# Optimization experiments

Measured on AMD Instinct MI355X. Metric: run time of the kernel, lower is better.

Reference implementation:

```python
import jax, jax.numpy as jnp
import numpy as np

NUM_FEATURES = 128
NUM_FILTERS = 128

def setup_inputs() -> dict:
    key = jax.random.key(0)
    k1, k2, k3, k4, k5 = jax.random.split(key, 5)
    B, N, F = 4, 2048, NUM_FEATURES
    x = jax.random.normal(k1, (B, N, F), dtype=jnp.float32)
    A = jax.random.normal(k2, (B, N, N), dtype=jnp.float32)
    # Conv1D(num_filters, kernel_size=1, use_bias=False) == per-node linear F -> filters
    W = jax.random.normal(k3, (F, NUM_FILTERS), dtype=jnp.float32) * (1.0 / np.sqrt(F))
    # self.a: Conv1D(1, kernel_size=1) with bias == linear filters -> 1 (shared for x_i and x_j)
    a_w = jax.random.normal(k4, (NUM_FILTERS, 1), dtype=jnp.float32) * (1.0 / np.sqrt(NUM_FILTERS))
    a_b = jax.random.normal(k5, (1,), dtype=jnp.float32) * 0.01
    bias = jnp.zeros((NUM_FILTERS,), dtype=jnp.float32)
    return {"x": x, "A": A, "W": W, "a_w": a_w, "a_b": a_b, "bias": bias}

def reference(x, A, W, a_w, a_b, bias):
    # project features: [B,N,F] @ [F,Ff] -> [B,N,Ff]
    h = jnp.einsum('bnf,fg->bng', x, W)
    # shared attention projection (x_i and x_j use the same layer): [B,N,1]
    s = jnp.einsum('bng,go->bno', h, a_w) + a_b
    # additive scores s_i + s_j^T -> [B,N,N]
    e = s + jnp.swapaxes(s, 1, 2)
    e = jnp.where(e >= 0, e, 0.2 * e)  # LeakyReLU(0.2)
    attn = jax.nn.softmax(e + A, axis=-1)
    out = jnp.einsum('bij,bjg->big', attn, h) + bias
    return out
```

## Files before the change

kernel.cpp:

```cpp
#include <hip/hip_runtime.h>
#include <hip/hip_bf16.h>
#include <stdint.h>

#define BB 4
#define NN 2048
#define FF 128

typedef __attribute__((ext_vector_type(8))) short bf16x8;
typedef __attribute__((ext_vector_type(4))) float f32x4;

__device__ inline unsigned pk_bf16(float a, float b) {
    union { float f; unsigned u; } x, y;
    x.f = a; y.f = b;
    unsigned xu = x.u + (0x7fffu + ((x.u >> 16) & 1u));
    unsigned yu = y.u + (0x7fffu + ((y.u >> 16) & 1u));
    return (xu >> 16) | (yu & 0xffff0000u);
}

#define XT_P 136
#define WT_P 136

__global__ __launch_bounds__(256) void k1_proj(
    const float* __restrict__ x, const float* __restrict__ W,
    const float* __restrict__ a_w, const float* __restrict__ a_b,
    uint16_t* __restrict__ Ht, float* __restrict__ s_out)
{
    __shared__ uint16_t xt[16 * XT_P];
    __shared__ uint16_t Wt[128 * WT_P];
    __shared__ float sredw[4 * 16];

    const int t = threadIdx.x;
    const int w = t >> 6, l = t & 63;
    const int m16 = l & 15, q = l >> 4;
    const int b = blockIdx.x >> 7;
    const int n0 = (blockIdx.x & 127) << 4;

    const int c4 = (t & 31) * 4, kh = (t >> 5) * 16;
    float4 wr0[8], wr1[8];
    #pragma unroll
    for (int kk = 0; kk < 8; ++kk) {
        const int k = kh + 2 * kk;
        wr0[kk] = *(const float4*)(W + (size_t)k * 128 + c4);
        wr1[kk] = *(const float4*)(W + (size_t)(k + 1) * 128 + c4);
    }
    {
        const int row = t >> 4, c0 = (t & 15) * 8;
        const float* xr = x + ((size_t)(b * NN + n0 + row)) * FF + c0;
        const float4 v0 = *(const float4*)xr;
        const float4 v1 = *(const float4*)(xr + 4);
        unsigned* dst = (unsigned*)(xt + row * XT_P + c0);
        dst[0] = pk_bf16(v0.x, v0.y); dst[1] = pk_bf16(v0.z, v0.w);
        dst[2] = pk_bf16(v1.x, v1.y); dst[3] = pk_bf16(v1.z, v1.w);
    }
    #pragma unroll
    for (int kk = 0; kk < 8; ++kk) {
        const int k = kh + 2 * kk;
        *(unsigned*)(Wt + (c4 + 0) * WT_P + k) = pk_bf16(wr0[kk].x, wr1[kk].x);
        *(unsigned*)(Wt + (c4 + 1) * WT_P + k) = pk_bf16(wr0[kk].y, wr1[kk].y);
        *(unsigned*)(Wt + (c4 + 2) * WT_P + k) = pk_bf16(wr0[kk].z, wr1[kk].z);
        *(unsigned*)(Wt + (c4 + 3) * WT_P + k) = pk_bf16(wr0[kk].w, wr1[kk].w);
    }
    const int g0 = (2 * w) * 16 + m16, g1 = (2 * w + 1) * 16 + m16;
    const float aw0 = a_w[g0], aw1 = a_w[g1];
    __syncthreads();

    f32x4 acc0 = {}, acc1 = {};
    bf16x8 af[4];
    #pragma unroll
    for (int dk = 0; dk < 4; ++dk)
        af[dk] = *(const bf16x8*)(xt + m16 * XT_P + dk * 32 + q * 8);
    #pragma unroll
    for (int dk = 0; dk < 4; ++dk) {
        bf16x8 b0 = *(const bf16x8*)(Wt + g0 * WT_P + dk * 32 + q * 8);
        bf16x8 b1 = *(const bf16x8*)(Wt + g1 * WT_P + dk * 32 + q * 8);
        acc0 = __builtin_amdgcn_mfma_f32_16x16x32_bf16(af[dk], b0, acc0, 0, 0, 0);
        acc1 = __builtin_amdgcn_mfma_f32_16x16x32_bf16(af[dk], b1, acc1, 0, 0, 0);
    }

    float sp[4];
    #pragma unroll
    for (int r = 0; r < 4; ++r) sp[r] = acc0[r] * aw0 + acc1[r] * aw1;
    #pragma unroll
    for (int off = 1; off < 16; off <<= 1)
        #pragma unroll
        for (int r = 0; r < 4; ++r) sp[r] += __shfl_xor(sp[r], off, 64);
    if (m16 == 0) {
        #pragma unroll
        for (int r = 0; r < 4; ++r) sredw[w * 16 + q * 4 + r] = sp[r];
    }
    {
        uint2 o0 = { pk_bf16(acc0[0], acc0[1]), pk_bf16(acc0[2], acc0[3]) };
        uint2 o1 = { pk_bf16(acc1[0], acc1[1]), pk_bf16(acc1[2], acc1[3]) };
        *(uint2*)(Ht + ((size_t)(b * 128 + g0)) * NN + n0 + q * 4) = o0;
        *(uint2*)(Ht + ((size_t)(b * 128 + g1)) * NN + n0 + q * 4) = o1;
    }
    __syncthreads();
    if (t < 16)
        s_out[b * NN + n0 + t] = sredw[t] + sredw[16 + t] + sredw[32 + t] + sredw[48 + t] + a_b[0];
}

#define JS 8
#define IRND 8

__global__ __launch_bounds__(256, 2) void k2_attn(
    const float* __restrict__ A, const uint16_t* __restrict__ Ht,
    const float* __restrict__ s, uint16_t* __restrict__ po,
    float* __restrict__ prs)
{
    __shared__ float Opw[4][16 * 132];
    __shared__ float rsw[4][16];

    const int t = threadIdx.x;
    const int w = t >> 6, l = t & 63;
    const int m16 = l & 15, q = l >> 4;

    const int bx = blockIdx.x;
    const int js = bx & 7;
    const int is = (bx >> 3) & 15;
    const int b  = bx >> 7;
    const int j0 = js * 256;
    const int ibase = is * 128;

    const float* sb = s + b * NN;
    const float* Ab = A + (size_t)b * NN * NN;
    const uint16_t* Hb = Ht + (size_t)b * FF * NN;

    const int jc0 = j0 + w * 32 + q * 8;
    const int jc1 = j0 + (w + 4) * 32 + q * 8;

    float4 sj00 = *(const float4*)(sb + jc0);
    float4 sj01 = *(const float4*)(sb + jc0 + 4);
    float4 sj10 = *(const float4*)(sb + jc1);
    float4 sj11 = *(const float4*)(sb + jc1 + 4);

    bf16x8 hf0[8], hf1[8];
    #pragma unroll
    for (int gt = 0; gt < 8; ++gt) {
        const uint16_t* hp = Hb + (size_t)(gt * 16 + m16) * NN;
        hf0[gt] = *(const bf16x8*)(hp + jc0);
        hf1[gt] = *(const bf16x8*)(hp + jc1);
    }

    const float* Ar = Ab + (size_t)(ibase + m16) * NN;
    float4 a00 = *(const float4*)(Ar + jc0);
    float4 a01 = *(const float4*)(Ar + jc0 + 4);
    float4 a10 = *(const float4*)(Ar + jc1);
    float4 a11 = *(const float4*)(Ar + jc1 + 4);
    float si = sb[ibase + m16];

    const size_t slice = (size_t)(js * BB + b);

    for (int r = 0; r < IRND; ++r) {
        const int i0r = ibase + r * 16;
        const int i0n = ibase + ((r + 1) & (IRND - 1)) * 16;

        const float* An = Ab + (size_t)(i0n + m16) * NN;
        float4 n00 = *(const float4*)(An + jc0);
        float4 n01 = *(const float4*)(An + jc0 + 4);
        float4 n10 = *(const float4*)(An + jc1);
        float4 n11 = *(const float4*)(An + jc1 + 4);
        const float sin_ = sb[i0n + m16];

        const float svv[16] = {sj00.x,sj00.y,sj00.z,sj00.w, sj01.x,sj01.y,sj01.z,sj01.w,
                               sj10.x,sj10.y,sj10.z,sj10.w, sj11.x,sj11.y,sj11.z,sj11.w};
        const float avv[16] = {a00.x,a00.y,a00.z,a00.w, a01.x,a01.y,a01.z,a01.w,
                               a10.x,a10.y,a10.z,a10.w, a11.x,a11.y,a11.z,a11.w};
        float pv[16]; float rs = 0.f;
        #pragma unroll
        for (int j = 0; j < 16; ++j) {
            float e = si + svv[j];
            e = fmaxf(e, 0.2f * e);
            pv[j] = __expf(e + avv[j]);
            rs += pv[j];
        }
        union { unsigned u[4]; bf16x8 v; } fa0, fa1;
        #pragma unroll
        for (int j = 0; j < 4; ++j) {
            fa0.u[j] = pk_bf16(pv[2 * j], pv[2 * j + 1]);
            fa1.u[j] = pk_bf16(pv[8 + 2 * j], pv[9 + 2 * j]);
        }

        f32x4 acc[8];
        #pragma unroll
        for (int gt = 0; gt < 8; ++gt) {
            f32x4 z = {0.f, 0.f, 0.f, 0.f};
            z = __builtin_amdgcn_mfma_f32_16x16x32_bf16(fa0.v, hf0[gt], z, 0, 0, 0);
            acc[gt] = __builtin_amdgcn_mfma_f32_16x16x32_bf16(fa1.v, hf1[gt], z, 0, 0, 0);
        }

        rs += __shfl_xor(rs, 16, 64);
        rs += __shfl_xor(rs, 32, 64);
        if (q == 0) rsw[w][m16] = rs;

        #pragma unroll
        for (int gt = 0; gt < 8; ++gt)
            #pragma unroll
            for (int rr = 0; rr < 4; ++rr)
                Opw[w][(q * 4 + rr) * 132 + gt * 16 + m16] = acc[gt][rr];
        asm volatile("s_waitcnt lgkmcnt(0)\n\ts_barrier" ::: "memory");

        {
            const int row = t >> 4, k8 = (t & 15) * 8;
            float v[8] = {0.f,0.f,0.f,0.f,0.f,0.f,0.f,0.f};
            #pragma unroll
            for (int sl = 0; sl < 4; ++sl) {
                float4 u0 = *(const float4*)&Opw[sl][row * 132 + k8];
                float4 u1 = *(const float4*)&Opw[sl][row * 132 + k8 + 4];
                v[0] += u0.x; v[1] += u0.y; v[2] += u0.z; v[3] += u0.w;
                v[4] += u1.x; v[5] += u1.y; v[6] += u1.z; v[7] += u1.w;
            }
            unsigned* op = (unsigned*)(po + ((slice * NN + i0r + row) * FF + k8));
            op[0] = pk_bf16(v[0], v[1]); op[1] = pk_bf16(v[2], v[3]);
            op[2] = pk_bf16(v[4], v[5]); op[3] = pk_bf16(v[6], v[7]);
            if (t < 16)
                prs[slice * NN + i0r + t] = rsw[0][t] + rsw[1][t] + rsw[2][t] + rsw[3][t];
        }
        asm volatile("s_waitcnt lgkmcnt(0)\n\ts_barrier" ::: "memory");

        a00 = n00; a01 = n01; a10 = n10; a11 = n11; si = sin_;
    }
}

__global__ __launch_bounds__(256) void k3_red(
    const uint16_t* __restrict__ po, const float* __restrict__ prs,
    const float* __restrict__ bias, float* __restrict__ out)
{
    const int idx = blockIdx.x * 256 + threadIdx.x;
    const int g = idx & 127;
    const int i = (idx >> 7) & (NN - 1);
    const int b = idx >> 18;
    float sum = 0.f, rsum = 0.f;
    #pragma unroll
    for (int js = 0; js < JS; ++js) {
        const size_t base = (size_t)(js * BB + b) * NN + i;
        union { unsigned u; float f; } cv;
        cv.u = ((unsigned)po[base * FF + g]) << 16;
        sum += cv.f;
        rsum += prs[base];
    }
    out[idx] = sum / rsum + bias[g];
}

extern "C" void kernel_launch(void* const* d_in, const int* in_sizes, int n_in,
                              void* d_out, int out_size, void* d_ws, size_t ws_size,
                              hipStream_t stream) {
    const float* x    = (const float*)d_in[0];
    const float* A    = (const float*)d_in[1];
    const float* W    = (const float*)d_in[2];
    const float* a_w  = (const float*)d_in[3];
    const float* a_b  = (const float*)d_in[4];
    const float* bias = (const float*)d_in[5];
    float* out = (float*)d_out;

    char* ws = (char*)d_ws;
    uint16_t* Ht = (uint16_t*)ws;
    float* s = (float*)(ws + 2 * 1024 * 1024);
    uint16_t* po = (uint16_t*)(ws + 2 * 1024 * 1024 + 65536);
    float* prs = (float*)(ws + 2 * 1024 * 1024 + 65536 + (size_t)JS * BB * NN * FF * 2);

    k1_proj<<<BB * (NN / 16), 256, 0, stream>>>(x, W, a_w, a_b, Ht, s);
    k2_attn<<<JS * 16 * BB, 256, 0, stream>>>(A, Ht, s, po, prs);
    k3_red<<<(BB * NN * FF) / 256, 256, 0, stream>>>(po, prs, bias, out);
}
```

Baseline: 126.7 us.

## Give each attention block full j range and fuse final reduction, drop k3

Changes the attention kernel split. Each block used to own a 256-column j-slice and 128 rows of i, writing bf16 partials that a third kernel reduced. Each block now owns 16 rows of i across the full j range and accumulates in MFMA registers, then normalizes, adds bias and writes fp32 output directly. This removes the partial-sum workspace traffic, the third launch and the per-round barriers. In exchange the block reloads the H fragments for every j chunk instead of keeping them resident, so H is read 8x more often (from L2). There is also no softmax max subtraction, same as before.

After: 138.7 us. +9.4%, slower.

```diff
diff --git a/kernel.cpp b/kernel.cpp
--- a/kernel.cpp
+++ b/kernel.cpp
@@ -99,13 +99,10 @@
         s_out[b * NN + n0 + t] = sredw[t] + sredw[16 + t] + sredw[32 + t] + sredw[48 + t] + a_b[0];
 }
 
-#define JS 8
-#define IRND 8
-
 __global__ __launch_bounds__(256, 2) void k2_attn(
     const float* __restrict__ A, const uint16_t* __restrict__ Ht,
-    const float* __restrict__ s, uint16_t* __restrict__ po,
-    float* __restrict__ prs)
+    const float* __restrict__ s, const float* __restrict__ bias,
+    float* __restrict__ out)
 {
     __shared__ float Opw[4][16 * 132];
     __shared__ float rsw[4][16];
@@ -114,58 +111,64 @@
     const int w = t >> 6, l = t & 63;
     const int m16 = l & 15, q = l >> 4;
 
-    const int bx = blockIdx.x;
-    const int js = bx & 7;
-    const int is = (bx >> 3) & 15;
-    const int b  = bx >> 7;
-    const int j0 = js * 256;
-    const int ibase = is * 128;
+    const int is = blockIdx.x & 127;
+    const int b  = blockIdx.x >> 7;
+    const int ibase = is * 16;
 
     const float* sb = s + b * NN;
     const float* Ab = A + (size_t)b * NN * NN;
     const uint16_t* Hb = Ht + (size_t)b * FF * NN;
 
-    const int jc0 = j0 + w * 32 + q * 8;
-    const int jc1 = j0 + (w + 4) * 32 + q * 8;
-
-    float4 sj00 = *(const float4*)(sb + jc0);
-    float4 sj01 = *(const float4*)(sb + jc0 + 4);
-    float4 sj10 = *(const float4*)(sb + jc1);
-    float4 sj11 = *(const float4*)(sb + jc1 + 4);
-
-    bf16x8 hf0[8], hf1[8];
-    #pragma unroll
-    for (int gt = 0; gt < 8; ++gt) {
-        const uint16_t* hp = Hb + (size_t)(gt * 16 + m16) * NN;
-        hf0[gt] = *(const bf16x8*)(hp + jc0);
-        hf1[gt] = *(const bf16x8*)(hp + jc1);
-    }
-
+    const float si = sb[ibase + m16];
     const float* Ar = Ab + (size_t)(ibase + m16) * NN;
-    float4 a00 = *(const float4*)(Ar + jc0);
-    float4 a01 = *(const float4*)(Ar + jc0 + 4);
-    float4 a10 = *(const float4*)(Ar + jc1);
-    float4 a11 = *(const float4*)(Ar + jc1 + 4);
-    float si = sb[ibase + m16];
-
-    const size_t slice = (size_t)(js * BB + b);
-
-    for (int r = 0; r < IRND; ++r) {
-        const int i0r = ibase + r * 16;
-        const int i0n = ibase + ((r + 1) & (IRND - 1)) * 16;
-
-        const float* An = Ab + (size_t)(i0n + m16) * NN;
-        float4 n00 = *(const float4*)(An + jc0);
-        float4 n01 = *(const float4*)(An + jc0 + 4);
-        float4 n10 = *(const float4*)(An + jc1);
-        float4 n11 = *(const float4*)(An + jc1 + 4);
-        const float sin_ = sb[i0n + m16];
+
+    const int co = w * 32 + q * 8;
+
+    float4 a00 = *(const float4*)(Ar + co);
+    float4 a01 = *(const float4*)(Ar + co + 4);
+    float4 a10 = *(const float4*)(Ar + co + 128);
+    float4 a11 = *(const float4*)(Ar + co + 132);
+    float4 sj00 = *(const float4*)(sb + co);
+    float4 sj01 = *(const float4*)(sb + co + 4);
+    float4 sj10 = *(const float4*)(sb + co + 128);
+    float4 sj11 = *(const float4*)(sb + co + 132);
+
+    f32x4 acc[8];
+    #pragma unroll
+    for (int gt = 0; gt < 8; ++gt) acc[gt] = (f32x4){0.f, 0.f, 0.f, 0.f};
+    float rs = 0.f;
+
+    #pragma unroll
+    for (int r = 0; r < 8; ++r) {
+        const int jc0 = r * 256 + co;
+        const int jc1 = jc0 + 128;
+
+        bf16x8 hf0[8], hf1[8];
+        #pragma unroll
+        for (int gt = 0; gt < 8; ++gt) {
+            const uint16_t* hp = Hb + (size_t)(gt * 16 + m16) * NN;
+            hf0[gt] = *(const bf16x8*)(hp + jc0);
+            hf1[gt] = *(const bf16x8*)(hp + jc1);
+        }
+
+        float4 n00, n01, n10, n11, t00, t01, t10, t11;
+        if (r < 7) {
+            const int jn = jc0 + 256;
+            n00 = *(const float4*)(Ar + jn);
+            n01 = *(const float4*)(Ar + jn + 4);
+            n10 = *(const float4*)(Ar + jn + 128);
+            n11 = *(const float4*)(Ar + jn + 132);
+            t00 = *(const float4*)(sb + jn);
+            t01 = *(const float4*)(sb + jn + 4);
+            t10 = *(const float4*)(sb + jn + 128);
+            t11 = *(const float4*)(sb + jn + 132);
+        }
 
         const float svv[16] = {sj00.x,sj00.y,sj00.z,sj00.w, sj01.x,sj01.y,sj01.z,sj01.w,
                                sj10.x,sj10.y,sj10.z,sj10.w, sj11.x,sj11.y,sj11.z,sj11.w};
         const float avv[16] = {a00.x,a00.y,a00.z,a00.w, a01.x,a01.y,a01.z,a01.w,
                                a10.x,a10.y,a10.z,a10.w, a11.x,a11.y,a11.z,a11.w};
-        float pv[16]; float rs = 0.f;
+        float pv[16];
         #pragma unroll
         for (int j = 0; j < 16; ++j) {
             float e = si + svv[j];
@@ -180,65 +183,48 @@
             fa1.u[j] = pk_bf16(pv[8 + 2 * j], pv[9 + 2 * j]);
         }
 
-        f32x4 acc[8];
         #pragma unroll
         for (int gt = 0; gt < 8; ++gt) {
-            f32x4 z = {0.f, 0.f, 0.f, 0.f};
-            z = __builtin_amdgcn_mfma_f32_16x16x32_bf16(fa0.v, hf0[gt], z, 0, 0, 0);
-            acc[gt] = __builtin_amdgcn_mfma_f32_16x16x32_bf16(fa1.v, hf1[gt], z, 0, 0, 0);
-        }
-
-        rs += __shfl_xor(rs, 16, 64);
-        rs += __shfl_xor(rs, 32, 64);
-        if (q == 0) rsw[w][m16] = rs;
-
-        #pragma unroll
-        for (int gt = 0; gt < 8; ++gt)
-            #pragma unroll
-            for (int rr = 0; rr < 4; ++rr)
-                Opw[w][(q * 4 + rr) * 132 + gt * 16 + m16] = acc[gt][rr];
-        asm volatile("s_waitcnt lgkmcnt(0)\n\ts_barrier" ::: "memory");
-
-        {
-            const int row = t >> 4, k8 = (t & 15) * 8;
-            float v[8] = {0.f,0.f,0.f,0.f,0.f,0.f,0.f,0.f};
-            #pragma unroll
-            for (int sl = 0; sl < 4; ++sl) {
-                float4 u0 = *(const float4*)&Opw[sl][row * 132 + k8];
-                float4 u1 = *(const float4*)&Opw[sl][row * 132 + k8 + 4];
-                v[0] += u0.x; v[1] += u0.y; v[2] += u0.z; v[3] += u0.w;
-                v[4] += u1.x; v[5] += u1.y; v[6] += u1.z; v[7] += u1.w;
-            }
-            unsigned* op = (unsigned*)(po + ((slice * NN + i0r + row) * FF + k8));
-            op[0] = pk_bf16(v[0], v[1]); op[1] = pk_bf16(v[2], v[3]);
-            op[2] = pk_bf16(v[4], v[5]); op[3] = pk_bf16(v[6], v[7]);
-            if (t < 16)
-                prs[slice * NN + i0r + t] = rsw[0][t] + rsw[1][t] + rsw[2][t] + rsw[3][t];
-        }
-        asm volatile("s_waitcnt lgkmcnt(0)\n\ts_barrier" ::: "memory");
-
-        a00 = n00; a01 = n01; a10 = n10; a11 = n11; si = sin_;
-    }
-}
-
-__global__ __launch_bounds__(256) void k3_red(
-    const uint16_t* __restrict__ po, const float* __restrict__ prs,
-    const float* __restrict__ bias, float* __restrict__ out)
-{
-    const int idx = blockIdx.x * 256 + threadIdx.x;
-    const int g = idx & 127;
-    const int i = (idx >> 7) & (NN - 1);
-    const int b = idx >> 18;
-    float sum = 0.f, rsum = 0.f;
-    #pragma unroll
-    for (int js = 0; js < JS; ++js) {
-        const size_t base = (size_t)(js * BB + b) * NN + i;
-        union { unsigned u; float f; } cv;
-        cv.u = ((unsigned)po[base * FF + g]) << 16;
-        sum += cv.f;
-        rsum += prs[base];
-    }
-    out[idx] = sum / rsum + bias[g];
+            acc[gt] = __builtin_amdgcn_mfma_f32_16x16x32_bf16(fa0.v, hf0[gt], acc[gt], 0, 0, 0);
+            acc[gt] = __builtin_amdgcn_mfma_f32_16x16x32_bf16(fa1.v, hf1[gt], acc[gt], 0, 0, 0);
+        }
+
+        if (r < 7) {
+            a00 = n00; a01 = n01; a10 = n10; a11 = n11;
+            sj00 = t00; sj01 = t01; sj10 = t10; sj11 = t11;
+        }
+    }
+
+    rs += __shfl_xor(rs, 16, 64);
+    rs += __shfl_xor(rs, 32, 64);
+    if (q == 0) rsw[w][m16] = rs;
+    #pragma unroll
+    for (int gt = 0; gt < 8; ++gt)
+        #pragma unroll
+        for (int rr = 0; rr < 4; ++rr)
+            Opw[w][(q * 4 + rr) * 132 + gt * 16 + m16] = acc[gt][rr];
+    __syncthreads();
+
+    {
+        const int row = t >> 4, k8 = (t & 15) * 8;
+        float v[8] = {0.f,0.f,0.f,0.f,0.f,0.f,0.f,0.f};
+        #pragma unroll
+        for (int sl = 0; sl < 4; ++sl) {
+            float4 u0 = *(const float4*)&Opw[sl][row * 132 + k8];
+            float4 u1 = *(const float4*)&Opw[sl][row * 132 + k8 + 4];
+            v[0] += u0.x; v[1] += u0.y; v[2] += u0.z; v[3] += u0.w;
+            v[4] += u1.x; v[5] += u1.y; v[6] += u1.z; v[7] += u1.w;
+        }
+        const float rst = rsw[0][row] + rsw[1][row] + rsw[2][row] + rsw[3][row];
+        const float inv = 1.0f / rst;
+        const float4 b0 = *(const float4*)(bias + k8);
+        const float4 b1 = *(const float4*)(bias + k8 + 4);
+        float4 o0 = { v[0]*inv + b0.x, v[1]*inv + b0.y, v[2]*inv + b0.z, v[3]*inv + b0.w };
+        float4 o1 = { v[4]*inv + b1.x, v[5]*inv + b1.y, v[6]*inv + b1.z, v[7]*inv + b1.w };
+        float* op = out + ((size_t)(b * NN + ibase + row)) * FF + k8;
+        *(float4*)op = o0;
+        *(float4*)(op + 4) = o1;
+    }
 }
 
 extern "C" void kernel_launch(void* const* d_in, const int* in_sizes, int n_in,
@@ -255,10 +241,7 @@
     char* ws = (char*)d_ws;
     uint16_t* Ht = (uint16_t*)ws;
     float* s = (float*)(ws + 2 * 1024 * 1024);
-    uint16_t* po = (uint16_t*)(ws + 2 * 1024 * 1024 + 65536);
-    float* prs = (float*)(ws + 2 * 1024 * 1024 + 65536 + (size_t)JS * BB * NN * FF * 2);
 
     k1_proj<<<BB * (NN / 16), 256, 0, stream>>>(x, W, a_w, a_b, Ht, s);
-    k2_attn<<<JS * 16 * BB, 256, 0, stream>>>(A, Ht, s, po, prs);
-    k3_red<<<(BB * NN * FF) / 256, 256, 0, stream>>>(po, prs, bias, out);
-}
+    k2_attn<<<128 * BB, 256, 0, stream>>>(A, Ht, s, bias, out);
+}
```

## Halve i-rows per attention block and vectorize the final reduction

Applied to the files above, without the earlier changes.

The attention kernel now processes 4 row rounds of 16 (64 rows) per block instead of 8 (128 rows), doubling the grid to 1024 blocks for better occupancy and load balance across CUs. This costs twice as many reloads of the per-block H fragments. The reduction kernel now handles 8 features per thread with 16-byte loads and stores, multiplies by a reciprocal instead of dividing, and launches one eighth as many threads. The odd 'acc[gt] = z' expression inside the MFMA call is redundant but harmless.

After: 128.0 us. No clear change (+1.0%).

```diff
diff --git a/kernel.cpp b/kernel.cpp
--- a/kernel.cpp
+++ b/kernel.cpp
@@ -100,7 +100,7 @@
 }
 
 #define JS 8
-#define IRND 8
+#define IRND 4
 
 __global__ __launch_bounds__(256, 2) void k2_attn(
     const float* __restrict__ A, const uint16_t* __restrict__ Ht,
@@ -116,10 +116,10 @@
 
     const int bx = blockIdx.x;
     const int js = bx & 7;
-    const int is = (bx >> 3) & 15;
-    const int b  = bx >> 7;
+    const int is = (bx >> 3) & 31;
+    const int b  = bx >> 8;
     const int j0 = js * 256;
-    const int ibase = is * 128;
+    const int ibase = is * 64;
 
     const float* sb = s + b * NN;
     const float* Ab = A + (size_t)b * NN * NN;
@@ -185,7 +185,7 @@
         for (int gt = 0; gt < 8; ++gt) {
             f32x4 z = {0.f, 0.f, 0.f, 0.f};
             z = __builtin_amdgcn_mfma_f32_16x16x32_bf16(fa0.v, hf0[gt], z, 0, 0, 0);
-            acc[gt] = __builtin_amdgcn_mfma_f32_16x16x32_bf16(fa1.v, hf1[gt], z, 0, 0, 0);
+            acc[gt] = __builtin_amdgcn_mfma_f32_16x16x32_bf16(fa1.v, hf1[gt], acc[gt] = z, 0, 0, 0);
         }
 
         rs += __shfl_xor(rs, 16, 64);
@@ -225,20 +225,36 @@
     const uint16_t* __restrict__ po, const float* __restrict__ prs,
     const float* __restrict__ bias, float* __restrict__ out)
 {
-    const int idx = blockIdx.x * 256 + threadIdx.x;
-    const int g = idx & 127;
-    const int i = (idx >> 7) & (NN - 1);
-    const int b = idx >> 18;
-    float sum = 0.f, rsum = 0.f;
+    const int gid = blockIdx.x * 256 + threadIdx.x;
+    const int g8 = (gid & 15) * 8;
+    const int i = (gid >> 4) & (NN - 1);
+    const int b = gid >> 15;
+
+    float v[8] = {0.f,0.f,0.f,0.f,0.f,0.f,0.f,0.f};
+    float rsum = 0.f;
     #pragma unroll
     for (int js = 0; js < JS; ++js) {
         const size_t base = (size_t)(js * BB + b) * NN + i;
-        union { unsigned u; float f; } cv;
-        cv.u = ((unsigned)po[base * FF + g]) << 16;
-        sum += cv.f;
+        const uint4 pv_ = *(const uint4*)(po + base * FF + g8);
+        const unsigned uu[4] = {pv_.x, pv_.y, pv_.z, pv_.w};
+        #pragma unroll
+        for (int k = 0; k < 4; ++k) {
+            union { unsigned u; float f; } lo, hi;
+            lo.u = uu[k] << 16;
+            hi.u = uu[k] & 0xffff0000u;
+            v[2 * k]     += lo.f;
+            v[2 * k + 1] += hi.f;
+        }
         rsum += prs[base];
     }
-    out[idx] = sum / rsum + bias[g];
+    const float inv = 1.0f / rsum;
+    const float4 b0 = *(const float4*)(bias + g8);
+    const float4 b1 = *(const float4*)(bias + g8 + 4);
+    float4 o0 = { v[0]*inv + b0.x, v[1]*inv + b0.y, v[2]*inv + b0.z, v[3]*inv + b0.w };
+    float4 o1 = { v[4]*inv + b1.x, v[5]*inv + b1.y, v[6]*inv + b1.z, v[7]*inv + b1.w };
+    float* op = out + ((size_t)(b * NN + i)) * FF + g8;
+    *(float4*)op = o0;
+    *(float4*)(op + 4) = o1;
 }
 
 extern "C" void kernel_launch(void* const* d_in, const int* in_sizes, int n_in,
@@ -259,6 +275,6 @@
     float* prs = (float*)(ws + 2 * 1024 * 1024 + 65536 + (size_t)JS * BB * NN * FF * 2);
 
     k1_proj<<<BB * (NN / 16), 256, 0, stream>>>(x, W, a_w, a_b, Ht, s);
-    k2_attn<<<JS * 16 * BB, 256, 0, stream>>>(A, Ht, s, po, prs);
-    k3_red<<<(BB * NN * FF) / 256, 256, 0, stream>>>(po, prs, bias, out);
-}
+    k2_attn<<<JS * 32 * BB, 256, 0, stream>>>(A, Ht, s, po, prs);
+    k3_red<<<(BB * NN * FF) / (256 * 8), 256, 0, stream>>>(po, prs, bias, out);
+}
```
